# Performance work log

Hardware: AMD Instinct MI355X
Metric: run time of the kernel (lower is better)

The kernel has to match this reference:

```python
import jax, jax.numpy as jnp
import numpy as np

B, C, H, W = 4, 128, 64, 64
HEADS, DH, MEM = 4, 32, 16
HID = HEADS * DH  # 128


def setup_inputs() -> dict:
    key = jax.random.key(0)
    k1, k2, k3, k4, k5 = jax.random.split(key, 5)
    return {
        "x": jax.random.normal(k1, (B, C, H, W), jnp.float32),
        "memory": jax.random.normal(k2, (1, C, 1, MEM), jnp.float32),
        "w_qkv": jax.random.normal(k3, (3 * HID, C), jnp.float32) * 0.05,  # conv1x1, bias=False
        "w_out": jax.random.normal(k4, (C, HID), jnp.float32) * 0.05,      # conv1x1 weight
        "b_out": jax.random.normal(k5, (C,), jnp.float32) * 0.01,          # conv1x1 bias
    }


def reference(x, memory, w_qkv, w_out, b_out):
    b, c, h, w = x.shape
    hw = h * w
    scale = DH ** -0.5

    # flatten spatial, append memory tokens along token axis
    x_flat = x.reshape(b, c, hw)                         # (b, c, hw)
    mem = jnp.broadcast_to(memory[:, :, 0, :], (b, c, MEM))
    x_ext = jnp.concatenate([x_flat, mem], axis=2)       # (b, c, n) n = hw + MEM

    # 1x1 conv QKV projection == channel matmul
    qkv = jnp.einsum('oc,bcn->bon', w_qkv, x_ext)        # (b, 3*HID, n)
    q, k, v = jnp.split(qkv, 3, axis=1)                  # each (b, HID, n)

    def to_heads(t):
        return t.reshape(b, HEADS, DH, -1)               # (b, h, d, n)

    q = to_heads(q) * scale
    k = to_heads(k)
    v = to_heads(v)

    sim = jnp.einsum('bhdi,bhdj->bhij', q, k)            # (b, h, n, n)
    attn = jax.nn.softmax(sim, axis=-1)                  # stable softmax (amax-sub inside)
    out = jnp.einsum('bhij,bhdj->bhid', attn, v)         # (b, h, n, d)

    out = out[:, :, :hw]                                 # drop memory-token queries
    out = out.transpose(0, 1, 3, 2).reshape(b, HID, h, w)  # b (h d) x y

    return jnp.einsum('oc,bchw->bohw', w_out, out) + b_out[None, :, None, None]
```

## Files before the change

kernel.cpp:

```cpp
#include <hip/hip_runtime.h>
#include <hip/hip_bf16.h>

constexpr int NQ   = 4096;
constexpr int NKV  = 4112;
constexpr int NP   = 4160;
constexpr int CDIM = 128;
constexpr int NSL  = 4;
constexpr float QSC = 0.17677669529663687f * 1.4426950408889634f;

typedef __attribute__((ext_vector_type(8)))  short bf16x8;
typedef __attribute__((ext_vector_type(4)))  short bf16x4;
typedef __attribute__((ext_vector_type(4)))  float f32x4;
typedef __attribute__((ext_vector_type(16))) float f32x16;

static __device__ __forceinline__ unsigned short bfbits(float f) {
  __hip_bfloat16 h = __float2bfloat16(f);
  return *reinterpret_cast<unsigned short*>(&h);
}
static __device__ __forceinline__ unsigned pk2(float a, float b) {
  return (unsigned)bfbits(a) | ((unsigned)bfbits(b) << 16);
}

__global__ __launch_bounds__(256) void k1_qkv(
    const float* __restrict__ x, const float* __restrict__ memry,
    const float* __restrict__ wqkv, const float* __restrict__ wout,
    __hip_bfloat16* __restrict__ Qt, __hip_bfloat16* __restrict__ Kt,
    __hip_bfloat16* __restrict__ Vt, __hip_bfloat16* __restrict__ Wb) {
  __shared__ __align__(16) __hip_bfloat16 xt[64][136];
  const int b  = blockIdx.y;
  const int zz = blockIdx.z;
  const int nb = blockIdx.x * 64;
  const int t  = threadIdx.x;
  const int wv = t >> 6, ln = t & 63;

  if (blockIdx.x == 0 && b == 0 && zz == 0) {
    for (int i = t; i < CDIM * CDIM; i += 256) Wb[i] = __float2bfloat16(wout[i]);
  }

  {
    const int n = nb + ln;
    #pragma unroll
    for (int i = 0; i < 16; ++i) {
      const int c = wv * 32 + 2 * i;
      float v0 = 0.f, v1 = 0.f;
      if (n < NQ)        { v0 = x[((size_t)b * CDIM + c) * NQ + n];
                           v1 = x[((size_t)b * CDIM + c + 1) * NQ + n]; }
      else if (n < NKV)  { v0 = memry[c * 16 + (n - NQ)];
                           v1 = memry[(c + 1) * 16 + (n - NQ)]; }
      *reinterpret_cast<unsigned*>(&xt[ln][c]) =
          (unsigned)bfbits(v0) | ((unsigned)bfbits(v1) << 16);
    }
  }
  __syncthreads();

  const int li = ln & 15, g = ln >> 4;
  bf16x8 xa[4][4];
  #pragma unroll
  for (int nt = 0; nt < 4; ++nt)
    #pragma unroll
    for (int k = 0; k < 4; ++k)
      xa[nt][k] = *reinterpret_cast<const bf16x8*>(&xt[nt * 16 + li][k * 32 + 8 * g]);

  #pragma unroll
  for (int oi = 0; oi < 3; ++oi) {
    const int ot = zz * 12 + wv * 3 + oi;
    bf16x8 wf[4];
    #pragma unroll
    for (int k = 0; k < 4; ++k) {
      const float* wp = &wqkv[(size_t)(ot * 16 + li) * CDIM + k * 32 + 8 * g];
      const float4 f0 = *reinterpret_cast<const float4*>(wp);
      const float4 f1 = *reinterpret_cast<const float4*>(wp + 4);
      bf16x8 wc;
      wc[0] = (short)bfbits(f0.x); wc[1] = (short)bfbits(f0.y);
      wc[2] = (short)bfbits(f0.z); wc[3] = (short)bfbits(f0.w);
      wc[4] = (short)bfbits(f1.x); wc[5] = (short)bfbits(f1.y);
      wc[6] = (short)bfbits(f1.z); wc[7] = (short)bfbits(f1.w);
      wf[k] = wc;
    }
    #pragma unroll
    for (int nt = 0; nt < 4; ++nt) {
      f32x4 a; a[0] = a[1] = a[2] = a[3] = 0.f;
      if (ot < 16) {
        #pragma unroll
        for (int k = 0; k < 4; ++k)
          a = __builtin_amdgcn_mfma_f32_16x16x32_bf16(xa[nt][k], wf[k], a, 0, 0, 0);
        const int o = ot * 16 + li;
        const int h = (o >> 5) & 3, d = o & 31;
        if (ot < 8) {
          #pragma unroll
          for (int r = 0; r < 4; ++r) {
            const int n = nb + nt * 16 + 4 * g + r;
            Qt[((size_t)(b * 4 + h) * NP + n) * 32 + d] = __float2bfloat16(a[r] * QSC);
          }
        } else {
          #pragma unroll
          for (int r = 0; r < 4; ++r) {
            const int n = nb + nt * 16 + 4 * g + r;
            Kt[((size_t)(b * 4 + h) * NP + n) * 32 + d] = __float2bfloat16(a[r]);
          }
        }
      } else {
        #pragma unroll
        for (int k = 0; k < 4; ++k)
          a = __builtin_amdgcn_mfma_f32_16x16x32_bf16(wf[k], xa[nt][k], a, 0, 0, 0);
        #pragma unroll
        for (int r = 0; r < 4; ++r) {
          const int o = ot * 16 + 4 * g + r;
          const int h = (o >> 5) & 3, d = o & 31;
          const int n = nb + nt * 16 + li;
          Vt[((size_t)(b * 4 + h) * 32 + d) * NP + n] = __float2bfloat16(a[r]);
        }
      }
    }
  }
}


#if __has_builtin(__builtin_amdgcn_mfma_f32_32x32x8bf16_1k)
#define HAS_PV8 1
#else
#define HAS_PV8 0
#endif

__global__ __launch_bounds__(256, 4) void k2_attn(
    const __hip_bfloat16* __restrict__ Qt, const __hip_bfloat16* __restrict__ Kt,
    const __hip_bfloat16* __restrict__ Vt, float* __restrict__ Pb,
    float* __restrict__ Lb) {
  __shared__ __align__(16) unsigned char smem[16384];

  const int wg  = blockIdx.x;
  const int xcd = wg & 7;
  const int i   = wg >> 3;
  const int bh  = 2 * xcd + (i & 1);
  const int sl  = (i >> 1) & 3;
  const int wv  = threadIdx.x >> 6, lane = threadIdx.x & 63;
  const int lq  = lane & 31, hi = lane >> 5;
  const int qb  = (i >> 3) * 128 + wv * 32;

  const bf16x8 qf0 = *reinterpret_cast<const bf16x8*>(
      Qt + ((size_t)bh * NP + qb + lq) * 32 + 8 * hi);
  const bf16x8 qf1 = *reinterpret_cast<const bf16x8*>(
      Qt + ((size_t)bh * NP + qb + lq) * 32 + 16 + 8 * hi);

  const int kb0 = sl * 1024;
  const __hip_bfloat16* Ksrc = Kt + ((size_t)bh * NP + kb0 + (wv >> 1) * 32 + lq) * 32
                                  + (wv & 1) * 16 + 8 * hi;
  const __hip_bfloat16* Vsrc = Vt + ((size_t)bh * 32 + lq) * NP + kb0 + wv * 16 + 8 * hi;
  const int dstoff = wv * 1024 + lane * 16;

  f32x16 acc0, acc1, z;
  #pragma unroll
  for (int q = 0; q < 16; ++q) { acc0[q] = 0.f; acc1[q] = 0.f; z[q] = 0.f; }
  float l0 = 0.f, l1 = 0.f, l2 = 0.f, l3 = 0.f;

  bf16x8 kreg = *reinterpret_cast<const bf16x8*>(Ksrc);
  bf16x8 vreg = *reinterpret_cast<const bf16x8*>(Vsrc);
  *reinterpret_cast<bf16x8*>(smem + dstoff)        = kreg;
  *reinterpret_cast<bf16x8*>(smem + 4096 + dstoff) = vreg;
  kreg = *reinterpret_cast<const bf16x8*>(Ksrc + 2048);
  vreg = *reinterpret_cast<const bf16x8*>(Vsrc + 64);

  for (int t = 0; t < 16; ++t) {
    __syncthreads();
    const int p = t & 1;
    if (t < 15) {
      unsigned char* nbuf = smem + (p ^ 1) * 8192;
      *reinterpret_cast<bf16x8*>(nbuf + dstoff)        = kreg;
      *reinterpret_cast<bf16x8*>(nbuf + 4096 + dstoff) = vreg;
      if (t < 14) {
        kreg = *reinterpret_cast<const bf16x8*>(Ksrc + (size_t)(t + 2) * 2048);
        vreg = *reinterpret_cast<const bf16x8*>(Vsrc + (t + 2) * 64);
      }
    }
    const __hip_bfloat16* kbuf = (const __hip_bfloat16*)(smem + p * 8192);
    const __hip_bfloat16* vbuf = (const __hip_bfloat16*)(smem + p * 8192 + 4096);

    #pragma unroll
    for (int st = 0; st < 2; ++st) {
      const bf16x8 kf0 = *reinterpret_cast<const bf16x8*>(kbuf + st * 1024 + lane * 8);
      const bf16x8 kf1 = *reinterpret_cast<const bf16x8*>(kbuf + st * 1024 + 512 + lane * 8);
      f32x16 s = __builtin_amdgcn_mfma_f32_32x32x16_bf16(kf0, qf0, z, 0, 0, 0);
      s = __builtin_amdgcn_mfma_f32_32x32x16_bf16(kf1, qf1, s, 0, 0, 0);
      float p_[16];
      #pragma unroll
      for (int r = 0; r < 16; ++r) p_[r] = __builtin_amdgcn_exp2f(s[r]);
      l0 += (p_[0] + p_[1]) + (p_[2] + p_[3]);
      l1 += (p_[4] + p_[5]) + (p_[6] + p_[7]);
      l2 += (p_[8] + p_[9]) + (p_[10] + p_[11]);
      l3 += (p_[12] + p_[13]) + (p_[14] + p_[15]);
#if HAS_PV8
      union UU { unsigned u[2]; bf16x4 v; };
      UU a0, a1, a2, a3;
      a0.u[0] = pk2(p_[0], p_[1]);   a0.u[1] = pk2(p_[2], p_[3]);
      a1.u[0] = pk2(p_[4], p_[5]);   a1.u[1] = pk2(p_[6], p_[7]);
      a2.u[0] = pk2(p_[8], p_[9]);   a2.u[1] = pk2(p_[10], p_[11]);
      a3.u[0] = pk2(p_[12], p_[13]); a3.u[1] = pk2(p_[14], p_[15]);
      const __hip_bfloat16* vb = vbuf + st * 1024 + lq * 8 + hi * 4;
      const bf16x4 vf0 = *reinterpret_cast<const bf16x4*>(vb);
      const bf16x4 vf1 = *reinterpret_cast<const bf16x4*>(vb + 256);
      const bf16x4 vf2 = *reinterpret_cast<const bf16x4*>(vb + 512);
      const bf16x4 vf3 = *reinterpret_cast<const bf16x4*>(vb + 768);
      acc0 = __builtin_amdgcn_mfma_f32_32x32x8bf16_1k(a0.v, vf0, acc0, 0, 0, 0);
      acc0 = __builtin_amdgcn_mfma_f32_32x32x8bf16_1k(a1.v, vf1, acc0, 0, 0, 0);
      acc1 = __builtin_amdgcn_mfma_f32_32x32x8bf16_1k(a2.v, vf2, acc1, 0, 0, 0);
      acc1 = __builtin_amdgcn_mfma_f32_32x32x8bf16_1k(a3.v, vf3, acc1, 0, 0, 0);
#else
      unsigned a0u0 = pk2(p_[0], p_[1]),   a0u1 = pk2(p_[2], p_[3]);
      unsigned a1u0 = pk2(p_[4], p_[5]),   a1u1 = pk2(p_[6], p_[7]);
      unsigned a2u0 = pk2(p_[8], p_[9]),   a2u1 = pk2(p_[10], p_[11]);
      unsigned a3u0 = pk2(p_[12], p_[13]), a3u1 = pk2(p_[14], p_[15]);
      union U8 { unsigned u[4]; bf16x8 v; };
      const bf16x8 vh0 = *reinterpret_cast<const bf16x8*>(vbuf + (2 * st) * 512 + lane * 8);
      const bf16x8 vh1 = *reinterpret_cast<const bf16x8*>(vbuf + (2 * st + 1) * 512 + lane * 8);
      {
        const unsigned s0 = __shfl_xor(hi ? a0u0 : a1u0, 32, 64);
        const unsigned s1 = __shfl_xor(hi ? a0u1 : a1u1, 32, 64);
        U8 f;
        f.u[0] = hi ? s0 : a0u0; f.u[1] = hi ? s1 : a0u1;
        f.u[2] = hi ? a1u0 : s0; f.u[3] = hi ? a1u1 : s1;
        acc0 = __builtin_amdgcn_mfma_f32_32x32x16_bf16(f.v, vh0, acc0, 0, 0, 0);
      }
      {
        const unsigned s0 = __shfl_xor(hi ? a2u0 : a3u0, 32, 64);
        const unsigned s1 = __shfl_xor(hi ? a2u1 : a3u1, 32, 64);
        U8 f;
        f.u[0] = hi ? s0 : a2u0; f.u[1] = hi ? s1 : a2u1;
        f.u[2] = hi ? a3u0 : s0; f.u[3] = hi ? a3u1 : s1;
        acc1 = __builtin_amdgcn_mfma_f32_32x32x16_bf16(f.v, vh1, acc1, 0, 0, 0);
      }
#endif
    }
  }

  if (sl == NSL - 1) {
    const __hip_bfloat16* Kp   = Kt + (size_t)bh * NP * 32 + (size_t)lq * 32 + 8 * hi;
    const __hip_bfloat16* Vrow = Vt + ((size_t)bh * 32 + lq) * NP;
    const int kb = 4096;
    const bf16x8 kf0 = *reinterpret_cast<const bf16x8*>(Kp + (size_t)kb * 32);
    const bf16x8 kf1 = *reinterpret_cast<const bf16x8*>(Kp + (size_t)kb * 32 + 16);
    f32x16 s = __builtin_amdgcn_mfma_f32_32x32x16_bf16(kf0, qf0, z, 0, 0, 0);
    s = __builtin_amdgcn_mfma_f32_32x32x16_bf16(kf1, qf1, s, 0, 0, 0);
    float p_[8];
    #pragma unroll
    for (int r = 0; r < 8; ++r) p_[r] = __builtin_amdgcn_exp2f(s[r]);
    l0 += (p_[0] + p_[1]) + (p_[2] + p_[3]);
    l1 += (p_[4] + p_[5]) + (p_[6] + p_[7]);
#if HAS_PV8
    union UU { unsigned u[2]; bf16x4 v; };
    UU a0, a1;
    a0.u[0] = pk2(p_[0], p_[1]); a0.u[1] = pk2(p_[2], p_[3]);
    a1.u[0] = pk2(p_[4], p_[5]); a1.u[1] = pk2(p_[6], p_[7]);
    const bf16x4 vf0 = *reinterpret_cast<const bf16x4*>(Vrow + kb + 4 * hi);
    const bf16x4 vf1 = *reinterpret_cast<const bf16x4*>(Vrow + kb + 8 + 4 * hi);
    acc0 = __builtin_amdgcn_mfma_f32_32x32x8bf16_1k(a0.v, vf0, acc0, 0, 0, 0);
    acc0 = __builtin_amdgcn_mfma_f32_32x32x8bf16_1k(a1.v, vf1, acc0, 0, 0, 0);
#else
    unsigned a0u0 = pk2(p_[0], p_[1]), a0u1 = pk2(p_[2], p_[3]);
    unsigned a1u0 = pk2(p_[4], p_[5]), a1u1 = pk2(p_[6], p_[7]);
    union U8 { unsigned u[4]; bf16x8 v; };
    const unsigned s0 = __shfl_xor(hi ? a0u0 : a1u0, 32, 64);
    const unsigned s1 = __shfl_xor(hi ? a0u1 : a1u1, 32, 64);
    U8 f;
    f.u[0] = hi ? s0 : a0u0; f.u[1] = hi ? s1 : a0u1;
    f.u[2] = hi ? a1u0 : s0; f.u[3] = hi ? a1u1 : s1;
    const bf16x8 vf = *reinterpret_cast<const bf16x8*>(Vrow + kb + 8 * hi);
    acc0 = __builtin_amdgcn_mfma_f32_32x32x16_bf16(f.v, vf, acc0, 0, 0, 0);
#endif
  }

  float* Pp = Pb + (((size_t)sl * 16 + bh) * NQ + qb) * 32;
  #pragma unroll
  for (int r = 0; r < 16; ++r) {
    const int q = (r & 3) + 8 * (r >> 2) + 4 * hi;
    Pp[(size_t)q * 32 + lq] = acc0[r] + acc1[r];
  }
  float lsum = (l0 + l1) + (l2 + l3);
  lsum += __shfl_xor(lsum, 32, 64);
  if (hi == 0)
    Lb[((size_t)sl * 16 + bh) * NQ + qb + lq] = lsum;
}

__global__ __launch_bounds__(256) void k2b_combine(
    const float* __restrict__ Pb, const float* __restrict__ Lb,
    __hip_bfloat16* __restrict__ att) {
  constexpr size_t PS = (size_t)16 * NQ * 32;
  constexpr size_t LS = (size_t)16 * NQ;
  const int wg  = blockIdx.x;
  const int xcd = wg & 7;
  const int i   = wg >> 3;
  const int bh  = 2 * xcd + (i & 1);
  const int j   = i >> 1;
  const int u   = j * 256 + threadIdx.x;
  const int q   = u >> 3;
  const int d0  = (u & 7) * 4;
  const size_t qi = (size_t)bh * NQ + q;

  float l = 0.f;
  #pragma unroll
  for (int s = 0; s < NSL; ++s) l += Lb[s * LS + qi];
  const float inv = 1.f / l;

  float4 o = make_float4(0.f, 0.f, 0.f, 0.f);
  #pragma unroll
  for (int s = 0; s < NSL; ++s) {
    const float4 f = *reinterpret_cast<const float4*>(Pb + s * PS + qi * 32 + d0);
    o.x += f.x; o.y += f.y; o.z += f.z; o.w += f.w;
  }
  *reinterpret_cast<uint2*>(att + qi * 32 + d0) =
      make_uint2(pk2(o.x * inv, o.y * inv), pk2(o.z * inv, o.w * inv));
}

__global__ __launch_bounds__(256) void k3_proj(
    const __hip_bfloat16* __restrict__ att, const __hip_bfloat16* __restrict__ Wb,
    const float* __restrict__ bout, float* __restrict__ out) {
  const int b = blockIdx.y, nb = blockIdx.x * 32;
  const int wv = threadIdx.x >> 6, lane = threadIdx.x & 63;
  const int li = lane & 15, g = lane >> 4;

  bf16x8 wf[2][4];
  float bo[2][4];
  #pragma unroll
  for (int tt = 0; tt < 2; ++tt) {
    const int ot = 2 * wv + tt;
    #pragma unroll
    for (int k = 0; k < 4; ++k)
      wf[tt][k] = *reinterpret_cast<const bf16x8*>(
          &Wb[(size_t)(ot * 16 + li) * CDIM + k * 32 + 8 * g]);
    #pragma unroll
    for (int r = 0; r < 4; ++r) bo[tt][r] = bout[ot * 16 + 4 * g + r];
  }
  #pragma unroll
  for (int nt = 0; nt < 2; ++nt) {
    bf16x8 bfr[4];
    #pragma unroll
    for (int k = 0; k < 4; ++k)
      bfr[k] = *reinterpret_cast<const bf16x8*>(
          &att[(((size_t)(b * 4 + k)) * NQ + nb + nt * 16 + li) * 32 + 8 * g]);
    #pragma unroll
    for (int tt = 0; tt < 2; ++tt) {
      f32x4 a; a[0] = a[1] = a[2] = a[3] = 0.f;
      #pragma unroll
      for (int k = 0; k < 4; ++k)
        a = __builtin_amdgcn_mfma_f32_16x16x32_bf16(wf[tt][k], bfr[k], a, 0, 0, 0);
      const int ot = 2 * wv + tt;
      #pragma unroll
      for (int r = 0; r < 4; ++r)
        out[((size_t)b * CDIM + ot * 16 + 4 * g + r) * NQ + nb + nt * 16 + li] =
            a[r] + bo[tt][r];
    }
  }
}

extern "C" void kernel_launch(void* const* d_in, const int* in_sizes, int n_in,
                              void* d_out, int out_size, void* d_ws, size_t ws_size,
                              hipStream_t stream) {
  const float* x    = (const float*)d_in[0];
  const float* memp = (const float*)d_in[1];
  const float* wqkv = (const float*)d_in[2];
  const float* wout = (const float*)d_in[3];
  const float* bout = (const float*)d_in[4];
  float* out = (float*)d_out;

  char* ws = (char*)d_ws;
  const size_t SZ  = (size_t)16 * NP * 32 * 2;
  const size_t PSZ = (size_t)NSL * 16 * NQ * 32 * 4;
  const size_t LSZ = (size_t)NSL * 16 * NQ * 4;
  const size_t ASZ = (size_t)16 * NQ * 32 * 2;
  __hip_bfloat16* Qt  = (__hip_bfloat16*)(ws);
  __hip_bfloat16* Kt  = (__hip_bfloat16*)(ws + SZ);
  __hip_bfloat16* Vt  = (__hip_bfloat16*)(ws + 2 * SZ);
  float*          Pbf = (float*)(ws + 3 * SZ);
  float*          Lbf = (float*)(ws + 3 * SZ + PSZ);
  __hip_bfloat16* att = (__hip_bfloat16*)(ws + 3 * SZ + PSZ + LSZ);
  __hip_bfloat16* Wb  = (__hip_bfloat16*)(ws + 3 * SZ + PSZ + LSZ + ASZ);

  hipLaunchKernelGGL(k1_qkv, dim3(65, 4, 2), dim3(256), 0, stream,
                     x, memp, wqkv, wout, Qt, Kt, Vt, Wb);
  hipLaunchKernelGGL(k2_attn, dim3(2048), dim3(256), 0, stream,
                     Qt, Kt, Vt, Pbf, Lbf);
  hipLaunchKernelGGL(k2b_combine, dim3(2048), dim3(256), 0, stream, Pbf, Lbf, att);
  hipLaunchKernelGGL(k3_proj, dim3(128, 4), dim3(256), 0, stream, att, Wb, bout, out);
}
```

Measured before the change: 94.62 us.

## Process two 32-query tiles per wave to reuse K/V LDS fragments

Each wave in the attention kernel now handles 64 queries (two 32-row tiles) and reuses every K and V fragment read from LDS for both, halving the grid to 1024 blocks. The V staging layout in shared memory is rearranged so each PV fragment is a contiguous 8-byte read, and the exp/pack/PV logic is factored into a helper. The aim is to halve LDS and global K/V traffic per query. In exchange, register pressure rises from the second accumulator and Q fragments, and fewer blocks may reduce occupancy and latency hiding.

```diff
diff --git a/kernel.cpp b/kernel.cpp
--- a/kernel.cpp
+++ b/kernel.cpp
@@ -122,6 +122,71 @@
 #define HAS_PV8 0
 #endif
 
+#if HAS_PV8
+__device__ __forceinline__ void half32(
+    const bf16x8& kf0, const bf16x8& kf1,
+    const bf16x4& vf0, const bf16x4& vf1, const bf16x4& vf2, const bf16x4& vf3,
+    const bf16x8& q0, const bf16x8& q1, const f32x16& z,
+    f32x16& acc, float& l0, float& l1, float& l2, float& l3) {
+  f32x16 s = __builtin_amdgcn_mfma_f32_32x32x16_bf16(kf0, q0, z, 0, 0, 0);
+  s = __builtin_amdgcn_mfma_f32_32x32x16_bf16(kf1, q1, s, 0, 0, 0);
+  float p[16];
+  #pragma unroll
+  for (int r = 0; r < 16; ++r) p[r] = __builtin_amdgcn_exp2f(s[r]);
+  l0 += (p[0] + p[1]) + (p[2] + p[3]);
+  l1 += (p[4] + p[5]) + (p[6] + p[7]);
+  l2 += (p[8] + p[9]) + (p[10] + p[11]);
+  l3 += (p[12] + p[13]) + (p[14] + p[15]);
+  union UU { unsigned u[2]; bf16x4 v; };
+  UU a0, a1, a2, a3;
+  a0.u[0] = pk2(p[0], p[1]);   a0.u[1] = pk2(p[2], p[3]);
+  a1.u[0] = pk2(p[4], p[5]);   a1.u[1] = pk2(p[6], p[7]);
+  a2.u[0] = pk2(p[8], p[9]);   a2.u[1] = pk2(p[10], p[11]);
+  a3.u[0] = pk2(p[12], p[13]); a3.u[1] = pk2(p[14], p[15]);
+  acc = __builtin_amdgcn_mfma_f32_32x32x8bf16_1k(a0.v, vf0, acc, 0, 0, 0);
+  acc = __builtin_amdgcn_mfma_f32_32x32x8bf16_1k(a1.v, vf1, acc, 0, 0, 0);
+  acc = __builtin_amdgcn_mfma_f32_32x32x8bf16_1k(a2.v, vf2, acc, 0, 0, 0);
+  acc = __builtin_amdgcn_mfma_f32_32x32x8bf16_1k(a3.v, vf3, acc, 0, 0, 0);
+}
+#else
+__device__ __forceinline__ void half32_fb(
+    const bf16x8& kf0, const bf16x8& kf1,
+    const bf16x8& vh0, const bf16x8& vh1, int hi,
+    const bf16x8& q0, const bf16x8& q1, const f32x16& z,
+    f32x16& acc, float& l0, float& l1, float& l2, float& l3) {
+  f32x16 s = __builtin_amdgcn_mfma_f32_32x32x16_bf16(kf0, q0, z, 0, 0, 0);
+  s = __builtin_amdgcn_mfma_f32_32x32x16_bf16(kf1, q1, s, 0, 0, 0);
+  float p[16];
+  #pragma unroll
+  for (int r = 0; r < 16; ++r) p[r] = __builtin_amdgcn_exp2f(s[r]);
+  l0 += (p[0] + p[1]) + (p[2] + p[3]);
+  l1 += (p[4] + p[5]) + (p[6] + p[7]);
+  l2 += (p[8] + p[9]) + (p[10] + p[11]);
+  l3 += (p[12] + p[13]) + (p[14] + p[15]);
+  unsigned a0u0 = pk2(p[0], p[1]),   a0u1 = pk2(p[2], p[3]);
+  unsigned a1u0 = pk2(p[4], p[5]),   a1u1 = pk2(p[6], p[7]);
+  unsigned a2u0 = pk2(p[8], p[9]),   a2u1 = pk2(p[10], p[11]);
+  unsigned a3u0 = pk2(p[12], p[13]), a3u1 = pk2(p[14], p[15]);
+  union U8 { unsigned u[4]; bf16x8 v; };
+  {
+    const unsigned s0 = __shfl_xor(hi ? a0u0 : a1u0, 32, 64);
+    const unsigned s1 = __shfl_xor(hi ? a0u1 : a1u1, 32, 64);
+    U8 f;
+    f.u[0] = hi ? s0 : a0u0; f.u[1] = hi ? s1 : a0u1;
+    f.u[2] = hi ? a1u0 : s0; f.u[3] = hi ? a1u1 : s1;
+    acc = __builtin_amdgcn_mfma_f32_32x32x16_bf16(f.v, vh0, acc, 0, 0, 0);
+  }
+  {
+    const unsigned s0 = __shfl_xor(hi ? a2u0 : a3u0, 32, 64);
+    const unsigned s1 = __shfl_xor(hi ? a2u1 : a3u1, 32, 64);
+    U8 f;
+    f.u[0] = hi ? s0 : a2u0; f.u[1] = hi ? s1 : a2u1;
+    f.u[2] = hi ? a3u0 : s0; f.u[3] = hi ? a3u1 : s1;
+    acc = __builtin_amdgcn_mfma_f32_32x32x16_bf16(f.v, vh1, acc, 0, 0, 0);
+  }
+}
+#endif
+
 __global__ __launch_bounds__(256, 4) void k2_attn(
     const __hip_bfloat16* __restrict__ Qt, const __hip_bfloat16* __restrict__ Kt,
     const __hip_bfloat16* __restrict__ Vt, float* __restrict__ Pb,
@@ -133,30 +198,48 @@
   const int i   = wg >> 3;
   const int bh  = 2 * xcd + (i & 1);
   const int sl  = (i >> 1) & 3;
+  const int iq  = i >> 3;
   const int wv  = threadIdx.x >> 6, lane = threadIdx.x & 63;
   const int lq  = lane & 31, hi = lane >> 5;
-  const int qb  = (i >> 3) * 128 + wv * 32;
-
-  const bf16x8 qf0 = *reinterpret_cast<const bf16x8*>(
-      Qt + ((size_t)bh * NP + qb + lq) * 32 + 8 * hi);
-  const bf16x8 qf1 = *reinterpret_cast<const bf16x8*>(
-      Qt + ((size_t)bh * NP + qb + lq) * 32 + 16 + 8 * hi);
+  const int qbase = iq * 256 + wv * 64;
+
+  const bf16x8 qA0 = *reinterpret_cast<const bf16x8*>(
+      Qt + ((size_t)bh * NP + qbase + lq) * 32 + 8 * hi);
+  const bf16x8 qA1 = *reinterpret_cast<const bf16x8*>(
+      Qt + ((size_t)bh * NP + qbase + lq) * 32 + 16 + 8 * hi);
+  const bf16x8 qB0 = *reinterpret_cast<const bf16x8*>(
+      Qt + ((size_t)bh * NP + qbase + 32 + lq) * 32 + 8 * hi);
+  const bf16x8 qB1 = *reinterpret_cast<const bf16x8*>(
+      Qt + ((size_t)bh * NP + qbase + 32 + lq) * 32 + 16 + 8 * hi);
 
   const int kb0 = sl * 1024;
   const __hip_bfloat16* Ksrc = Kt + ((size_t)bh * NP + kb0 + (wv >> 1) * 32 + lq) * 32
                                   + (wv & 1) * 16 + 8 * hi;
   const __hip_bfloat16* Vsrc = Vt + ((size_t)bh * 32 + lq) * NP + kb0 + wv * 16 + 8 * hi;
-  const int dstoff = wv * 1024 + lane * 16;
-
-  f32x16 acc0, acc1, z;
-  #pragma unroll
-  for (int q = 0; q < 16; ++q) { acc0[q] = 0.f; acc1[q] = 0.f; z[q] = 0.f; }
-  float l0 = 0.f, l1 = 0.f, l2 = 0.f, l3 = 0.f;
+  const int kdst = wv * 1024 + lane * 16;
+  const int vdst = (wv >> 1) * 2048 + ((wv & 1) * 2 + hi) * 512 + lq * 8;
+  const int rdv  = hi * 256 + lq * 8;
+
+  f32x16 accA, accB, z;
+  #pragma unroll
+  for (int q = 0; q < 16; ++q) { accA[q] = 0.f; accB[q] = 0.f; z[q] = 0.f; }
+  float la0 = 0.f, la1 = 0.f, la2 = 0.f, la3 = 0.f;
+  float lb0 = 0.f, lb1 = 0.f, lb2 = 0.f, lb3 = 0.f;
 
   bf16x8 kreg = *reinterpret_cast<const bf16x8*>(Ksrc);
   bf16x8 vreg = *reinterpret_cast<const bf16x8*>(Vsrc);
-  *reinterpret_cast<bf16x8*>(smem + dstoff)        = kreg;
-  *reinterpret_cast<bf16x8*>(smem + 4096 + dstoff) = vreg;
+
+#define WRITE_KV(basep)                                                        \
+  {                                                                            \
+    *reinterpret_cast<bf16x8*>((basep) + kdst) = kreg;                         \
+    bf16x4 vlo, vhi;                                                           \
+    vlo[0] = vreg[0]; vlo[1] = vreg[1]; vlo[2] = vreg[2]; vlo[3] = vreg[3];    \
+    vhi[0] = vreg[4]; vhi[1] = vreg[5]; vhi[2] = vreg[6]; vhi[3] = vreg[7];    \
+    *reinterpret_cast<bf16x4*>((basep) + 4096 + vdst)       = vlo;             \
+    *reinterpret_cast<bf16x4*>((basep) + 4096 + vdst + 256) = vhi;             \
+  }
+
+  WRITE_KV(smem)
   kreg = *reinterpret_cast<const bf16x8*>(Ksrc + 2048);
   vreg = *reinterpret_cast<const bf16x8*>(Vsrc + 64);
 
@@ -165,72 +248,40 @@
     const int p = t & 1;
     if (t < 15) {
       unsigned char* nbuf = smem + (p ^ 1) * 8192;
-      *reinterpret_cast<bf16x8*>(nbuf + dstoff)        = kreg;
-      *reinterpret_cast<bf16x8*>(nbuf + 4096 + dstoff) = vreg;
+      WRITE_KV(nbuf)
       if (t < 14) {
         kreg = *reinterpret_cast<const bf16x8*>(Ksrc + (size_t)(t + 2) * 2048);
         vreg = *reinterpret_cast<const bf16x8*>(Vsrc + (t + 2) * 64);
       }
     }
-    const __hip_bfloat16* kbuf = (const __hip_bfloat16*)(smem + p * 8192);
-    const __hip_bfloat16* vbuf = (const __hip_bfloat16*)(smem + p * 8192 + 4096);
+    const unsigned char* kbuf = smem + p * 8192;
+    const unsigned char* vbase = kbuf + 4096;
 
     #pragma unroll
     for (int st = 0; st < 2; ++st) {
-      const bf16x8 kf0 = *reinterpret_cast<const bf16x8*>(kbuf + st * 1024 + lane * 8);
-      const bf16x8 kf1 = *reinterpret_cast<const bf16x8*>(kbuf + st * 1024 + 512 + lane * 8);
-      f32x16 s = __builtin_amdgcn_mfma_f32_32x32x16_bf16(kf0, qf0, z, 0, 0, 0);
-      s = __builtin_amdgcn_mfma_f32_32x32x16_bf16(kf1, qf1, s, 0, 0, 0);
-      float p_[16];
-      #pragma unroll
-      for (int r = 0; r < 16; ++r) p_[r] = __builtin_amdgcn_exp2f(s[r]);
-      l0 += (p_[0] + p_[1]) + (p_[2] + p_[3]);
-      l1 += (p_[4] + p_[5]) + (p_[6] + p_[7]);
-      l2 += (p_[8] + p_[9]) + (p_[10] + p_[11]);
-      l3 += (p_[12] + p_[13]) + (p_[14] + p_[15]);
+      const bf16x8 kf0 = *reinterpret_cast<const bf16x8*>(kbuf + st * 2048 + lane * 16);
+      const bf16x8 kf1 = *reinterpret_cast<const bf16x8*>(kbuf + st * 2048 + 1024 + lane * 16);
 #if HAS_PV8
-      union UU { unsigned u[2]; bf16x4 v; };
-      UU a0, a1, a2, a3;
-      a0.u[0] = pk2(p_[0], p_[1]);   a0.u[1] = pk2(p_[2], p_[3]);
-      a1.u[0] = pk2(p_[4], p_[5]);   a1.u[1] = pk2(p_[6], p_[7]);
-      a2.u[0] = pk2(p_[8], p_[9]);   a2.u[1] = pk2(p_[10], p_[11]);
-      a3.u[0] = pk2(p_[12], p_[13]); a3.u[1] = pk2(p_[14], p_[15]);
-      const __hip_bfloat16* vb = vbuf + st * 1024 + lq * 8 + hi * 4;
-      const bf16x4 vf0 = *reinterpret_cast<const bf16x4*>(vb);
-      const bf16x4 vf1 = *reinterpret_cast<const bf16x4*>(vb + 256);
-      const bf16x4 vf2 = *reinterpret_cast<const bf16x4*>(vb + 512);
-      const bf16x4 vf3 = *reinterpret_cast<const bf16x4*>(vb + 768);
-      acc0 = __builtin_amdgcn_mfma_f32_32x32x8bf16_1k(a0.v, vf0, acc0, 0, 0, 0);
-      acc0 = __builtin_amdgcn_mfma_f32_32x32x8bf16_1k(a1.v, vf1, acc0, 0, 0, 0);
-      acc1 = __builtin_amdgcn_mfma_f32_32x32x8bf16_1k(a2.v, vf2, acc1, 0, 0, 0);
-      acc1 = __builtin_amdgcn_mfma_f32_32x32x8bf16_1k(a3.v, vf3, acc1, 0, 0, 0);
+      const unsigned char* vb = vbase + st * 2048;
+      const bf16x4 vf0 = *reinterpret_cast<const bf16x4*>(vb + rdv);
+      const bf16x4 vf1 = *reinterpret_cast<const bf16x4*>(vb + 512 + rdv);
+      const bf16x4 vf2 = *reinterpret_cast<const bf16x4*>(vb + 1024 + rdv);
+      const bf16x4 vf3 = *reinterpret_cast<const bf16x4*>(vb + 1536 + rdv);
+      half32(kf0, kf1, vf0, vf1, vf2, vf3, qA0, qA1, z, accA, la0, la1, la2, la3);
+      half32(kf0, kf1, vf0, vf1, vf2, vf3, qB0, qB1, z, accB, lb0, lb1, lb2, lb3);
 #else
-      unsigned a0u0 = pk2(p_[0], p_[1]),   a0u1 = pk2(p_[2], p_[3]);
-      unsigned a1u0 = pk2(p_[4], p_[5]),   a1u1 = pk2(p_[6], p_[7]);
-      unsigned a2u0 = pk2(p_[8], p_[9]),   a2u1 = pk2(p_[10], p_[11]);
-      unsigned a3u0 = pk2(p_[12], p_[13]), a3u1 = pk2(p_[14], p_[15]);
-      union U8 { unsigned u[4]; bf16x8 v; };
-      const bf16x8 vh0 = *reinterpret_cast<const bf16x8*>(vbuf + (2 * st) * 512 + lane * 8);
-      const bf16x8 vh1 = *reinterpret_cast<const bf16x8*>(vbuf + (2 * st + 1) * 512 + lane * 8);
-      {
-        const unsigned s0 = __shfl_xor(hi ? a0u0 : a1u0, 32, 64);
-        const unsigned s1 = __shfl_xor(hi ? a0u1 : a1u1, 32, 64);
-        U8 f;
-        f.u[0] = hi ? s0 : a0u0; f.u[1] = hi ? s1 : a0u1;
-        f.u[2] = hi ? a1u0 : s0; f.u[3] = hi ? a1u1 : s1;
-        acc0 = __builtin_amdgcn_mfma_f32_32x32x16_bf16(f.v, vh0, acc0, 0, 0, 0);
-      }
-      {
-        const unsigned s0 = __shfl_xor(hi ? a2u0 : a3u0, 32, 64);
-        const unsigned s1 = __shfl_xor(hi ? a2u1 : a3u1, 32, 64);
-        U8 f;
-        f.u[0] = hi ? s0 : a2u0; f.u[1] = hi ? s1 : a2u1;
-        f.u[2] = hi ? a3u0 : s0; f.u[3] = hi ? a3u1 : s1;
-        acc1 = __builtin_amdgcn_mfma_f32_32x32x16_bf16(f.v, vh1, acc1, 0, 0, 0);
-      }
+      const unsigned char* vb = vbase + st * 2048;
+      union { bf16x4 h[2]; bf16x8 w; } vh0, vh1;
+      vh0.h[0] = *reinterpret_cast<const bf16x4*>(vb + hi * 512 + lq * 8);
+      vh0.h[1] = *reinterpret_cast<const bf16x4*>(vb + hi * 512 + 256 + lq * 8);
+      vh1.h[0] = *reinterpret_cast<const bf16x4*>(vb + (2 + hi) * 512 + lq * 8);
+      vh1.h[1] = *reinterpret_cast<const bf16x4*>(vb + (2 + hi) * 512 + 256 + lq * 8);
+      half32_fb(kf0, kf1, vh0.w, vh1.w, hi, qA0, qA1, z, accA, la0, la1, la2, la3);
+      half32_fb(kf0, kf1, vh0.w, vh1.w, hi, qB0, qB1, z, accB, lb0, lb1, lb2, lb3);
 #endif
     }
   }
+#undef WRITE_KV
 
   if (sl == NSL - 1) {
     const __hip_bfloat16* Kp   = Kt + (size_t)bh * NP * 32 + (size_t)lq * 32 + 8 * hi;
@@ -238,46 +289,66 @@
     const int kb = 4096;
     const bf16x8 kf0 = *reinterpret_cast<const bf16x8*>(Kp + (size_t)kb * 32);
     const bf16x8 kf1 = *reinterpret_cast<const bf16x8*>(Kp + (size_t)kb * 32 + 16);
-    f32x16 s = __builtin_amdgcn_mfma_f32_32x32x16_bf16(kf0, qf0, z, 0, 0, 0);
-    s = __builtin_amdgcn_mfma_f32_32x32x16_bf16(kf1, qf1, s, 0, 0, 0);
-    float p_[8];
-    #pragma unroll
-    for (int r = 0; r < 8; ++r) p_[r] = __builtin_amdgcn_exp2f(s[r]);
-    l0 += (p_[0] + p_[1]) + (p_[2] + p_[3]);
-    l1 += (p_[4] + p_[5]) + (p_[6] + p_[7]);
 #if HAS_PV8
-    union UU { unsigned u[2]; bf16x4 v; };
-    UU a0, a1;
-    a0.u[0] = pk2(p_[0], p_[1]); a0.u[1] = pk2(p_[2], p_[3]);
-    a1.u[0] = pk2(p_[4], p_[5]); a1.u[1] = pk2(p_[6], p_[7]);
-    const bf16x4 vf0 = *reinterpret_cast<const bf16x4*>(Vrow + kb + 4 * hi);
-    const bf16x4 vf1 = *reinterpret_cast<const bf16x4*>(Vrow + kb + 8 + 4 * hi);
-    acc0 = __builtin_amdgcn_mfma_f32_32x32x8bf16_1k(a0.v, vf0, acc0, 0, 0, 0);
-    acc0 = __builtin_amdgcn_mfma_f32_32x32x8bf16_1k(a1.v, vf1, acc0, 0, 0, 0);
+    const bf16x4 vt0 = *reinterpret_cast<const bf16x4*>(Vrow + kb + 4 * hi);
+    const bf16x4 vt1 = *reinterpret_cast<const bf16x4*>(Vrow + kb + 8 + 4 * hi);
 #else
-    unsigned a0u0 = pk2(p_[0], p_[1]), a0u1 = pk2(p_[2], p_[3]);
-    unsigned a1u0 = pk2(p_[4], p_[5]), a1u1 = pk2(p_[6], p_[7]);
-    union U8 { unsigned u[4]; bf16x8 v; };
-    const unsigned s0 = __shfl_xor(hi ? a0u0 : a1u0, 32, 64);
-    const unsigned s1 = __shfl_xor(hi ? a0u1 : a1u1, 32, 64);
-    U8 f;
-    f.u[0] = hi ? s0 : a0u0; f.u[1] = hi ? s1 : a0u1;
-    f.u[2] = hi ? a1u0 : s0; f.u[3] = hi ? a1u1 : s1;
-    const bf16x8 vf = *reinterpret_cast<const bf16x8*>(Vrow + kb + 8 * hi);
-    acc0 = __builtin_amdgcn_mfma_f32_32x32x16_bf16(f.v, vf, acc0, 0, 0, 0);
+    const bf16x8 vt8 = *reinterpret_cast<const bf16x8*>(Vrow + kb + 8 * hi);
 #endif
-  }
-
-  float* Pp = Pb + (((size_t)sl * 16 + bh) * NQ + qb) * 32;
+    #pragma unroll
+    for (int hf = 0; hf < 2; ++hf) {
+      const bf16x8 q0 = hf ? qB0 : qA0;
+      const bf16x8 q1 = hf ? qB1 : qA1;
+      f32x16 s = __builtin_amdgcn_mfma_f32_32x32x16_bf16(kf0, q0, z, 0, 0, 0);
+      s = __builtin_amdgcn_mfma_f32_32x32x16_bf16(kf1, q1, s, 0, 0, 0);
+      float p_[8];
+      #pragma unroll
+      for (int r = 0; r < 8; ++r) p_[r] = __builtin_amdgcn_exp2f(s[r]);
+      const float s01 = (p_[0] + p_[1]) + (p_[2] + p_[3]);
+      const float s23 = (p_[4] + p_[5]) + (p_[6] + p_[7]);
+      if (hf) { lb0 += s01; lb1 += s23; } else { la0 += s01; la1 += s23; }
+#if HAS_PV8
+      union UU { unsigned u[2]; bf16x4 v; };
+      UU a0, a1;
+      a0.u[0] = pk2(p_[0], p_[1]); a0.u[1] = pk2(p_[2], p_[3]);
+      a1.u[0] = pk2(p_[4], p_[5]); a1.u[1] = pk2(p_[6], p_[7]);
+      if (hf) {
+        accB = __builtin_amdgcn_mfma_f32_32x32x8bf16_1k(a0.v, vt0, accB, 0, 0, 0);
+        accB = __builtin_amdgcn_mfma_f32_32x32x8bf16_1k(a1.v, vt1, accB, 0, 0, 0);
+      } else {
+        accA = __builtin_amdgcn_mfma_f32_32x32x8bf16_1k(a0.v, vt0, accA, 0, 0, 0);
+        accA = __builtin_amdgcn_mfma_f32_32x32x8bf16_1k(a1.v, vt1, accA, 0, 0, 0);
+      }
+#else
+      unsigned a0u0 = pk2(p_[0], p_[1]), a0u1 = pk2(p_[2], p_[3]);
+      unsigned a1u0 = pk2(p_[4], p_[5]), a1u1 = pk2(p_[6], p_[7]);
+      union U8 { unsigned u[4]; bf16x8 v; };
+      const unsigned s0 = __shfl_xor(hi ? a0u0 : a1u0, 32, 64);
+      const unsigned s1 = __shfl_xor(hi ? a0u1 : a1u1, 32, 64);
+      U8 f;
+      f.u[0] = hi ? s0 : a0u0; f.u[1] = hi ? s1 : a0u1;
+      f.u[2] = hi ? a1u0 : s0; f.u[3] = hi ? a1u1 : s1;
+      if (hf) accB = __builtin_amdgcn_mfma_f32_32x32x16_bf16(f.v, vt8, accB, 0, 0, 0);
+      else    accA = __builtin_amdgcn_mfma_f32_32x32x16_bf16(f.v, vt8, accA, 0, 0, 0);
+#endif
+    }
+  }
+
+  float* PpA = Pb + (((size_t)sl * 16 + bh) * NQ + qbase) * 32;
   #pragma unroll
   for (int r = 0; r < 16; ++r) {
     const int q = (r & 3) + 8 * (r >> 2) + 4 * hi;
-    Pp[(size_t)q * 32 + lq] = acc0[r] + acc1[r];
-  }
-  float lsum = (l0 + l1) + (l2 + l3);
-  lsum += __shfl_xor(lsum, 32, 64);
-  if (hi == 0)
-    Lb[((size_t)sl * 16 + bh) * NQ + qb + lq] = lsum;
+    PpA[(size_t)q * 32 + lq] = accA[r];
+    PpA[(size_t)(q + 32) * 32 + lq] = accB[r];
+  }
+  float lsA = (la0 + la1) + (la2 + la3);
+  float lsB = (lb0 + lb1) + (lb2 + lb3);
+  lsA += __shfl_xor(lsA, 32, 64);
+  lsB += __shfl_xor(lsB, 32, 64);
+  if (hi == 0) {
+    Lb[((size_t)sl * 16 + bh) * NQ + qbase + lq] = lsA;
+    Lb[((size_t)sl * 16 + bh) * NQ + qbase + 32 + lq] = lsB;
+  }
 }
 
 __global__ __launch_bounds__(256) void k2b_combine(
@@ -376,7 +447,7 @@
 
   hipLaunchKernelGGL(k1_qkv, dim3(65, 4, 2), dim3(256), 0, stream,
                      x, memp, wqkv, wout, Qt, Kt, Vt, Wb);
-  hipLaunchKernelGGL(k2_attn, dim3(2048), dim3(256), 0, stream,
+  hipLaunchKernelGGL(k2_attn, dim3(1024), dim3(256), 0, stream,
                      Qt, Kt, Vt, Pbf, Lbf);
   hipLaunchKernelGGL(k2b_combine, dim3(2048), dim3(256), 0, stream, Pbf, Lbf, att);
   hipLaunchKernelGGL(k3_proj, dim3(128, 4), dim3(256), 0, stream, att, Wb, bout, out);
```

New measurement: 119.1 us. 25.8% more time.
